# Kernel tuning notes

Hardware: AMD Instinct MI355X
Metric: run time of the kernel (lower is better)

The kernel has to match this reference:

```python
import jax, jax.numpy as jnp
import numpy as np

EPS = 1e-6
MAX_Q = 25.0
B, M, N, S = 1024, 8192, 32, 128


def setup_inputs() -> dict:
    key = jax.random.key(0)
    k = jax.random.split(key, 6)
    z = jax.random.normal(k[0], (B, N), jnp.float32) * 1e-3
    z_j = jax.random.uniform(k[1], (M, N), jnp.float32, -1e-3, 1e-3)
    vec_d_j = jax.random.uniform(k[2], (M, N), jnp.float32, -1e-3, 1e-3)
    T_hat_j = jax.random.uniform(k[3], (M, S), jnp.float32, -1e-3, 1e-3)
    alpha_j = jnp.ones((M,), jnp.float32)
    sigma_par = jax.random.uniform(k[4], (M,), jnp.float32, 0.9, 1.5)
    sigma_perp = jax.random.uniform(k[5], (M,), jnp.float32, 0.1, 0.8)
    return {"z": z, "z_j": z_j, "vec_d_j": vec_d_j, "T_hat_j": T_hat_j,
            "alpha_j": alpha_j, "sigma_par": sigma_par, "sigma_perp": sigma_perp}


def reference(z, z_j, vec_d_j, T_hat_j, alpha_j, sigma_par, sigma_perp):
    tiny = jnp.finfo(sigma_par.dtype).eps
    w_par = 1.0 / jnp.maximum(sigma_par, tiny) ** 2      # [M]
    w_perp = 1.0 / jnp.maximum(sigma_perp, tiny) ** 2    # [M]
    w_diff = w_par - w_perp                               # [M]

    dz = z[:, None, :] - z_j[None, :, :]                  # [B, M, N]
    dz_norm_sq = jnp.sum(dz * dz, axis=-1)                # [B, M]

    d_norm = jnp.linalg.norm(vec_d_j, axis=-1, keepdims=True)  # [M, 1]
    use_proj = (d_norm > EPS).astype(z.dtype)                   # [M, 1]
    b = jnp.where(d_norm > EPS, vec_d_j / d_norm, jnp.zeros_like(vec_d_j))  # [M, N]
    proj = jnp.einsum('bmn,mn->bm', dz, b) * use_proj[:, 0][None, :]        # [B, M]

    q_pos = w_perp[None, :] * dz_norm_sq + w_diff[None, :] * (proj * proj)  # [B, M]
    q_pos = jnp.minimum(q_pos, jnp.asarray(MAX_Q, dtype=z.dtype))

    gain = alpha_j[None, :] * jnp.exp(-jnp.pi * q_pos)    # [B, M]
    T = gain @ T_hat_j                                     # [B, S]
    return T
```

## Files before the change

kernel.cpp:

```cpp
#include <hip/hip_runtime.h>
#include <hip/hip_bf16.h>
#include <math.h>

#define B_SZ 1024
#define M_SZ 8192
#define N_SZ 32
#define S_SZ 128

#define MT   256
#define BT   64
#define NTHR 256

#define SG_STRIDE 264

typedef __bf16 bf16x8 __attribute__((ext_vector_type(8)));
typedef float  f32x4  __attribute__((ext_vector_type(4)));

#define NSPLIT 32
#define WS_TSWZ_BYTES  ((size_t)M_SZ * S_SZ * 2)
#define WS_PART_BYTES  ((size_t)NSPLIT * B_SZ * S_SZ * 4)
#define WS_NEED        (WS_TSWZ_BYTES + WS_PART_BYTES)

__global__ __launch_bounds__(256)
void prep_T_kernel(const float* __restrict__ T, char* __restrict__ Tswz)
{
    const int g    = blockIdx.x * 256 + threadIdx.x;
    const int mc   = g >> 9;
    const int ns   = (g >> 6) & 7;
    const int lane = g & 63;
    const int c    = lane & 15;
    const int q    = lane >> 4;
    const float* src = T + (size_t)(mc * 32 + q * 8) * S_SZ + ns * 16 + c;
    bf16x8 v;
    #pragma unroll
    for (int j = 0; j < 8; ++j) v[j] = (__bf16)src[(size_t)j * S_SZ];
    *(bf16x8*)(Tswz + (size_t)g * 16) = v;
}

__global__ __launch_bounds__(NTHR, 2)
void cpsf_mfma_kernel(const float* __restrict__ z,
                      const float* __restrict__ z_j,
                      const float* __restrict__ vec_d_j,
                      const char*  __restrict__ Tswz,
                      const float* __restrict__ alpha_j,
                      const float* __restrict__ sigma_par,
                      const float* __restrict__ sigma_perp,
                      float* __restrict__ ws_part)
{
    __shared__ __align__(16) float sZ[BT * N_SZ];
    __shared__ float sZn[BT];
    __shared__ __align__(16) __hip_bfloat16 sG[BT * SG_STRIDE];

    const int t     = threadIdx.x;
    const int mx    = blockIdx.x;
    const int m0    = mx * MT;
    const int bbase = blockIdx.y * BT;

    {
        const float4* z4 = (const float4*)z + (size_t)bbase * (N_SZ / 4);
        float4* s4 = (float4*)sZ;
        #pragma unroll
        for (int i = t; i < BT * N_SZ / 4; i += NTHR) s4[i] = z4[i];
    }

    const int m = m0 + t;
    float zj[N_SZ], dv[N_SZ];
    {
        const float4* a4 = (const float4*)(z_j     + (size_t)m * N_SZ);
        const float4* d4 = (const float4*)(vec_d_j + (size_t)m * N_SZ);
        #pragma unroll
        for (int i = 0; i < N_SZ / 4; ++i) {
            float4 av = a4[i], dw = d4[i];
            zj[4*i+0]=av.x; zj[4*i+1]=av.y; zj[4*i+2]=av.z; zj[4*i+3]=av.w;
            dv[4*i+0]=dw.x; dv[4*i+1]=dw.y; dv[4*i+2]=dw.z; dv[4*i+3]=dw.w;
        }
    }
    float zjn = 0.f, dnsq = 0.f, zjd = 0.f;
    #pragma unroll
    for (int n = 0; n < N_SZ; ++n) {
        zjn  += zj[n] * zj[n];
        dnsq += dv[n] * dv[n];
        zjd  += zj[n] * dv[n];
    }
    const float dn     = sqrtf(dnsq);
    const float inv_dn = (dn > 1e-6f) ? (1.0f / dn) : 0.0f;
    const float P0     = zjd * inv_dn;
    const float tiny   = 1.1920928955078125e-07f;
    const float sp  = fmaxf(sigma_par[m],  tiny);
    const float spp = fmaxf(sigma_perp[m], tiny);
    const float wpar  = 1.0f / (sp  * sp);
    const float wperp = 1.0f / (spp * spp);
    const float wdiff = wpar - wperp;
    const float Cc    = wperp * zjn;
    const float al    = alpha_j[m];

    __syncthreads();
    if (t < BT) {
        float s = 0.f;
        #pragma unroll
        for (int n = 0; n < N_SZ; ++n) { float v = sZ[t * N_SZ + n]; s += v * v; }
        sZn[t] = s;
    }
    __syncthreads();

    const float PI_F = 3.14159274101257324f;
    for (int b = 0; b < BT; ++b) {
        float s1 = 0.f, sd = 0.f;
        #pragma unroll
        for (int n = 0; n < N_SZ; ++n) {
            const float zv = sZ[b * N_SZ + n];
            s1 += zv * zj[n];
            sd += zv * dv[n];
        }
        const float p = sd * inv_dn - P0;
        float q = wperp * sZn[b] - 2.0f * wperp * s1 + Cc + wdiff * p * p;
        q = fminf(q, 25.0f);
        const float g = al * __expf(-PI_F * q);
        sG[b * SG_STRIDE + t] = __float2bfloat16(g);
    }
    __syncthreads();

    const int lane = t & 63;
    const int w    = t >> 6;
    const int q    = lane >> 4;
    const int c    = lane & 15;

    f32x4 acc[8];
    #pragma unroll
    for (int ns = 0; ns < 8; ++ns) acc[ns] = (f32x4){0.f, 0.f, 0.f, 0.f};

    const char* sGb = (const char*)sG + (size_t)(w * 16 + c) * (SG_STRIDE * 2);
    #pragma unroll
    for (int kc = 0; kc < MT / 32; ++kc) {
        bf16x8 a = *(const bf16x8*)(sGb + kc * 64 + q * 16);
        const int mc = mx * (MT / 32) + kc;
        #pragma unroll
        for (int ns = 0; ns < 8; ++ns) {
            bf16x8 b = *(const bf16x8*)(Tswz + ((size_t)(mc * 8 + ns) * 64 + lane) * 16);
            acc[ns] = __builtin_amdgcn_mfma_f32_16x16x32_bf16(a, b, acc[ns], 0, 0, 0);
        }
    }

    float* part = ws_part + (size_t)mx * (B_SZ * S_SZ)
                + (size_t)(bbase + w * 16 + q * 4) * S_SZ + c;
    #pragma unroll
    for (int ns = 0; ns < 8; ++ns)
        #pragma unroll
        for (int reg = 0; reg < 4; ++reg)
            part[(size_t)reg * S_SZ + ns * 16] = acc[ns][reg];
}

__global__ __launch_bounds__(256)
void reduce_kernel(const float* __restrict__ part, float* __restrict__ out)
{
    const int i = blockIdx.x * 256 + threadIdx.x;
    const f32x4* p = (const f32x4*)part;
    f32x4 s = p[i];
    #pragma unroll
    for (int sp = 1; sp < NSPLIT; ++sp) {
        f32x4 v = p[(size_t)sp * (B_SZ * S_SZ / 4) + i];
        s = s + v;
    }
    ((f32x4*)out)[i] = s;
}

#define SGF_STRIDE 68
__global__ __launch_bounds__(NTHR, 2)
void cpsf_fused_fallback(const float* __restrict__ z,
                         const float* __restrict__ z_j,
                         const float* __restrict__ vec_d_j,
                         const float* __restrict__ T_hat,
                         const float* __restrict__ alpha_j,
                         const float* __restrict__ sigma_par,
                         const float* __restrict__ sigma_perp,
                         float* __restrict__ out)
{
    __shared__ float sZ[BT * N_SZ];
    __shared__ float sZn[BT];
    __shared__ float sG[MT * SGF_STRIDE];

    const int t     = threadIdx.x;
    const int m0    = blockIdx.x * MT;
    const int bbase = blockIdx.y * BT;

    {
        const float4* z4 = (const float4*)z + (size_t)bbase * (N_SZ / 4);
        float4* s4 = (float4*)sZ;
        #pragma unroll
        for (int i = t; i < BT * N_SZ / 4; i += NTHR) s4[i] = z4[i];
    }
    const int m = m0 + t;
    float zj[N_SZ], dv[N_SZ];
    {
        const float4* a4 = (const float4*)(z_j     + (size_t)m * N_SZ);
        const float4* d4 = (const float4*)(vec_d_j + (size_t)m * N_SZ);
        #pragma unroll
        for (int i = 0; i < N_SZ / 4; ++i) {
            float4 av = a4[i], dw = d4[i];
            zj[4*i+0]=av.x; zj[4*i+1]=av.y; zj[4*i+2]=av.z; zj[4*i+3]=av.w;
            dv[4*i+0]=dw.x; dv[4*i+1]=dw.y; dv[4*i+2]=dw.z; dv[4*i+3]=dw.w;
        }
    }
    float zjn = 0.f, dnsq = 0.f, zjd = 0.f;
    #pragma unroll
    for (int n = 0; n < N_SZ; ++n) {
        zjn += zj[n]*zj[n]; dnsq += dv[n]*dv[n]; zjd += zj[n]*dv[n];
    }
    const float dn = sqrtf(dnsq);
    const float inv_dn = (dn > 1e-6f) ? (1.0f / dn) : 0.0f;
    const float P0 = zjd * inv_dn;
    const float tiny = 1.1920928955078125e-07f;
    const float sp  = fmaxf(sigma_par[m],  tiny);
    const float spp = fmaxf(sigma_perp[m], tiny);
    const float wperp = 1.0f / (spp * spp);
    const float wdiff = 1.0f / (sp * sp) - wperp;
    const float Cc = wperp * zjn;
    const float al = alpha_j[m];

    __syncthreads();
    if (t < BT) {
        float s = 0.f;
        #pragma unroll
        for (int n = 0; n < N_SZ; ++n) { float v = sZ[t*N_SZ+n]; s += v*v; }
        sZn[t] = s;
    }
    __syncthreads();

    const float PI_F = 3.14159274101257324f;
    for (int bq = 0; bq < BT / 4; ++bq) {
        float g[4];
        #pragma unroll
        for (int k = 0; k < 4; ++k) {
            const int b = bq*4 + k;
            float s1 = 0.f, sd = 0.f;
            #pragma unroll
            for (int n = 0; n < N_SZ; ++n) {
                const float zv = sZ[b*N_SZ+n];
                s1 += zv*zj[n]; sd += zv*dv[n];
            }
            const float p = sd*inv_dn - P0;
            float qv = wperp*sZn[b] - 2.0f*wperp*s1 + Cc + wdiff*p*p;
            qv = fminf(qv, 25.0f);
            g[k] = al * __expf(-PI_F*qv);
        }
        *(float4*)&sG[t*SGF_STRIDE + bq*4] = make_float4(g[0],g[1],g[2],g[3]);
    }
    __syncthreads();

    const int sg = t & 15, bg = t >> 4;
    const int b0 = bg*4, s0 = sg*8;
    float acc[4][8];
    #pragma unroll
    for (int i = 0; i < 4; ++i)
        #pragma unroll
        for (int j = 0; j < 8; ++j) acc[i][j] = 0.f;
    const float4* th4 = (const float4*)T_hat + (size_t)m0*(S_SZ/4) + sg*2;
    for (int mm = 0; mm < MT; ++mm) {
        const float4 g4 = *(const float4*)&sG[mm*SGF_STRIDE + b0];
        const float4 ta = th4[(size_t)mm*(S_SZ/4)];
        const float4 tb = th4[(size_t)mm*(S_SZ/4)+1];
        const float gg[4] = {g4.x,g4.y,g4.z,g4.w};
        const float tv[8] = {ta.x,ta.y,ta.z,ta.w,tb.x,tb.y,tb.z,tb.w};
        #pragma unroll
        for (int i = 0; i < 4; ++i)
            #pragma unroll
            for (int j = 0; j < 8; ++j) acc[i][j] += gg[i]*tv[j];
    }
    float* op = out + (size_t)(bbase + b0)*S_SZ + s0;
    #pragma unroll
    for (int i = 0; i < 4; ++i)
        #pragma unroll
        for (int j = 0; j < 8; ++j)
            unsafeAtomicAdd(&op[i*S_SZ + j], acc[i][j]);
}

extern "C" void kernel_launch(void* const* d_in, const int* in_sizes, int n_in,
                              void* d_out, int out_size, void* d_ws, size_t ws_size,
                              hipStream_t stream) {
    (void)in_sizes; (void)n_in; (void)out_size;

    const float* z          = (const float*)d_in[0];
    const float* z_j        = (const float*)d_in[1];
    const float* vec_d_j    = (const float*)d_in[2];
    const float* T_hat_j    = (const float*)d_in[3];
    const float* alpha_j    = (const float*)d_in[4];
    const float* sigma_par  = (const float*)d_in[5];
    const float* sigma_perp = (const float*)d_in[6];
    float* out = (float*)d_out;

    if (ws_size >= WS_NEED) {
        char*  Tswz = (char*)d_ws;
        float* part = (float*)((char*)d_ws + WS_TSWZ_BYTES);

        prep_T_kernel<<<dim3(M_SZ * S_SZ / (256 * 8)), 256, 0, stream>>>(T_hat_j, Tswz);

        dim3 grid(NSPLIT, B_SZ / BT);
        cpsf_mfma_kernel<<<grid, NTHR, 0, stream>>>(
            z, z_j, vec_d_j, Tswz, alpha_j, sigma_par, sigma_perp, part);

        reduce_kernel<<<dim3(B_SZ * S_SZ / (256 * 4)), 256, 0, stream>>>(part, out);
    } else {
        hipMemsetAsync(out, 0, (size_t)B_SZ * S_SZ * sizeof(float), stream);
        dim3 grid(M_SZ / MT, B_SZ / BT);
        cpsf_fused_fallback<<<grid, NTHR, 0, stream>>>(
            z, z_j, vec_d_j, T_hat_j, alpha_j, sigma_par, sigma_perp, out);
    }
}
```

Measured before the change: 107.3 us.

## Compute distance dot products with bf16 MFMA and precompute per-row constants in prep kernel

The prep kernel now also converts z, z_j and the normalised direction vectors to bf16 and precomputes the per-m constants (weights, norms, projection offset, alpha) and the per-b squared norms into workspace. The main kernel computes the z·z_j and z·d dot products with bf16 MFMA tiles instead of scalar FP32 loops over shared memory. The second GEMM is reorganised so each wave covers all 64 rows and a 32-column slice of S, and occupancy is raised to 4 blocks per CU. This removes the scalar VALU dot-product cost, but bf16 inputs to the quadratic form (a difference of near-equal terms) risk precision loss.

```diff
diff --git a/kernel.cpp b/kernel.cpp
--- a/kernel.cpp
+++ b/kernel.cpp
@@ -10,144 +10,191 @@
 #define MT   256
 #define BT   64
 #define NTHR 256
+#define NSPLIT 32
 
 #define SG_STRIDE 264
 
 typedef __bf16 bf16x8 __attribute__((ext_vector_type(8)));
 typedef float  f32x4  __attribute__((ext_vector_type(4)));
 
-#define NSPLIT 32
-#define WS_TSWZ_BYTES  ((size_t)M_SZ * S_SZ * 2)
-#define WS_PART_BYTES  ((size_t)NSPLIT * B_SZ * S_SZ * 4)
-#define WS_NEED        (WS_TSWZ_BYTES + WS_PART_BYTES)
+#define WS_TSWZ   ((size_t)0)
+#define WS_ZJBF   ((size_t)2 * 1024 * 1024)
+#define WS_DVBF   (WS_ZJBF + (size_t)M_SZ * N_SZ * 2)
+#define WS_MCONST (WS_DVBF + (size_t)M_SZ * N_SZ * 2)
+#define WS_ZBF    (WS_MCONST + (size_t)M_SZ * 8 * 4)
+#define WS_ZN     (WS_ZBF + (size_t)B_SZ * N_SZ * 2)
+#define WS_PART   ((size_t)4 * 1024 * 1024)
+#define WS_NEED   (WS_PART + (size_t)NSPLIT * B_SZ * S_SZ * 4)
 
 __global__ __launch_bounds__(256)
-void prep_T_kernel(const float* __restrict__ T, char* __restrict__ Tswz)
+void prep_kernel(const float* __restrict__ T,
+                 const float* __restrict__ z,
+                 const float* __restrict__ zj_in,
+                 const float* __restrict__ dv_in,
+                 const float* __restrict__ alpha_j,
+                 const float* __restrict__ sigma_par,
+                 const float* __restrict__ sigma_perp,
+                 char* __restrict__ ws)
 {
-    const int g    = blockIdx.x * 256 + threadIdx.x;
-    const int mc   = g >> 9;
-    const int ns   = (g >> 6) & 7;
-    const int lane = g & 63;
-    const int c    = lane & 15;
-    const int q    = lane >> 4;
-    const float* src = T + (size_t)(mc * 32 + q * 8) * S_SZ + ns * 16 + c;
-    bf16x8 v;
-    #pragma unroll
-    for (int j = 0; j < 8; ++j) v[j] = (__bf16)src[(size_t)j * S_SZ];
-    *(bf16x8*)(Tswz + (size_t)g * 16) = v;
-}
-
-__global__ __launch_bounds__(NTHR, 2)
-void cpsf_mfma_kernel(const float* __restrict__ z,
-                      const float* __restrict__ z_j,
-                      const float* __restrict__ vec_d_j,
-                      const char*  __restrict__ Tswz,
-                      const float* __restrict__ alpha_j,
-                      const float* __restrict__ sigma_par,
-                      const float* __restrict__ sigma_perp,
-                      float* __restrict__ ws_part)
+    const int bx = blockIdx.x;
+    const int t  = threadIdx.x;
+
+    if (bx < 512) {
+        const int g    = bx * 256 + t;
+        const int mc   = g >> 9;
+        const int ns   = (g >> 6) & 7;
+        const int lane = g & 63;
+        const int c    = lane & 15;
+        const int q    = lane >> 4;
+        const float* src = T + (size_t)(mc * 32 + q * 8) * S_SZ + ns * 16 + c;
+        bf16x8 v;
+        #pragma unroll
+        for (int j = 0; j < 8; ++j) v[j] = (__bf16)src[(size_t)j * S_SZ];
+        *(bf16x8*)(ws + WS_TSWZ + (size_t)g * 16) = v;
+    } else if (bx < 544) {
+        const int m = (bx - 512) * 256 + t;
+        float a[N_SZ], d[N_SZ];
+        const float4* a4 = (const float4*)(zj_in + (size_t)m * N_SZ);
+        const float4* d4 = (const float4*)(dv_in + (size_t)m * N_SZ);
+        #pragma unroll
+        for (int i = 0; i < N_SZ / 4; ++i) {
+            float4 av = a4[i], dw = d4[i];
+            a[4*i+0]=av.x; a[4*i+1]=av.y; a[4*i+2]=av.z; a[4*i+3]=av.w;
+            d[4*i+0]=dw.x; d[4*i+1]=dw.y; d[4*i+2]=dw.z; d[4*i+3]=dw.w;
+        }
+        float zjn = 0.f, dnsq = 0.f, zjd = 0.f;
+        #pragma unroll
+        for (int n = 0; n < N_SZ; ++n) {
+            zjn += a[n]*a[n]; dnsq += d[n]*d[n]; zjd += a[n]*d[n];
+        }
+        const float dn  = sqrtf(dnsq);
+        const float inv = (dn > 1e-6f) ? (1.0f / dn) : 0.0f;
+        __bf16* zjb = (__bf16*)(ws + WS_ZJBF) + (size_t)m * N_SZ;
+        __bf16* dvb = (__bf16*)(ws + WS_DVBF) + (size_t)m * N_SZ;
+        #pragma unroll
+        for (int i = 0; i < 4; ++i) {
+            bf16x8 vz, vd;
+            #pragma unroll
+            for (int j = 0; j < 8; ++j) {
+                vz[j] = (__bf16)a[i*8+j];
+                vd[j] = (__bf16)(d[i*8+j] * inv);
+            }
+            *(bf16x8*)(zjb + i*8) = vz;
+            *(bf16x8*)(dvb + i*8) = vd;
+        }
+        const float tiny = 1.1920928955078125e-07f;
+        const float sp  = fmaxf(sigma_par[m],  tiny);
+        const float spp = fmaxf(sigma_perp[m], tiny);
+        const float wperp = 1.0f / (spp * spp);
+        const float wdiff = 1.0f / (sp * sp) - wperp;
+        float* mc8 = (float*)(ws + WS_MCONST) + (size_t)m * 8;
+        *(f32x4*)mc8       = (f32x4){wperp, wperp * zjn, wdiff, zjd * inv};
+        *(f32x4*)(mc8 + 4) = (f32x4){alpha_j[m], 0.f, 0.f, 0.f};
+    } else {
+        const int b = (bx - 544) * 256 + t;
+        float v[N_SZ];
+        const float4* z4 = (const float4*)(z + (size_t)b * N_SZ);
+        #pragma unroll
+        for (int i = 0; i < N_SZ / 4; ++i) {
+            float4 w4 = z4[i];
+            v[4*i+0]=w4.x; v[4*i+1]=w4.y; v[4*i+2]=w4.z; v[4*i+3]=w4.w;
+        }
+        float zn = 0.f;
+        #pragma unroll
+        for (int n = 0; n < N_SZ; ++n) zn += v[n]*v[n];
+        __bf16* zb = (__bf16*)(ws + WS_ZBF) + (size_t)b * N_SZ;
+        #pragma unroll
+        for (int i = 0; i < 4; ++i) {
+            bf16x8 vz;
+            #pragma unroll
+            for (int j = 0; j < 8; ++j) vz[j] = (__bf16)v[i*8+j];
+            *(bf16x8*)(zb + i*8) = vz;
+        }
+        ((float*)(ws + WS_ZN))[b] = zn;
+    }
+}
+
+__global__ __launch_bounds__(NTHR, 4)
+void cpsf_main_kernel(const char* __restrict__ ws_ro, float* __restrict__ ws_part)
 {
-    __shared__ __align__(16) float sZ[BT * N_SZ];
-    __shared__ float sZn[BT];
-    __shared__ __align__(16) __hip_bfloat16 sG[BT * SG_STRIDE];
+    __shared__ __align__(16) __bf16 sG[BT * SG_STRIDE];
 
     const int t     = threadIdx.x;
+    const int lane  = t & 63;
+    const int w     = t >> 6;
+    const int q     = lane >> 4;
+    const int c     = lane & 15;
     const int mx    = blockIdx.x;
     const int m0    = mx * MT;
     const int bbase = blockIdx.y * BT;
 
-    {
-        const float4* z4 = (const float4*)z + (size_t)bbase * (N_SZ / 4);
-        float4* s4 = (float4*)sZ;
-        #pragma unroll
-        for (int i = t; i < BT * N_SZ / 4; i += NTHR) s4[i] = z4[i];
-    }
-
-    const int m = m0 + t;
-    float zj[N_SZ], dv[N_SZ];
-    {
-        const float4* a4 = (const float4*)(z_j     + (size_t)m * N_SZ);
-        const float4* d4 = (const float4*)(vec_d_j + (size_t)m * N_SZ);
-        #pragma unroll
-        for (int i = 0; i < N_SZ / 4; ++i) {
-            float4 av = a4[i], dw = d4[i];
-            zj[4*i+0]=av.x; zj[4*i+1]=av.y; zj[4*i+2]=av.z; zj[4*i+3]=av.w;
-            dv[4*i+0]=dw.x; dv[4*i+1]=dw.y; dv[4*i+2]=dw.z; dv[4*i+3]=dw.w;
-        }
-    }
-    float zjn = 0.f, dnsq = 0.f, zjd = 0.f;
-    #pragma unroll
-    for (int n = 0; n < N_SZ; ++n) {
-        zjn  += zj[n] * zj[n];
-        dnsq += dv[n] * dv[n];
-        zjd  += zj[n] * dv[n];
-    }
-    const float dn     = sqrtf(dnsq);
-    const float inv_dn = (dn > 1e-6f) ? (1.0f / dn) : 0.0f;
-    const float P0     = zjd * inv_dn;
-    const float tiny   = 1.1920928955078125e-07f;
-    const float sp  = fmaxf(sigma_par[m],  tiny);
-    const float spp = fmaxf(sigma_perp[m], tiny);
-    const float wpar  = 1.0f / (sp  * sp);
-    const float wperp = 1.0f / (spp * spp);
-    const float wdiff = wpar - wperp;
-    const float Cc    = wperp * zjn;
-    const float al    = alpha_j[m];
-
+    const __bf16* zbf   = (const __bf16*)(ws_ro + WS_ZBF);
+    const __bf16* zjbf  = (const __bf16*)(ws_ro + WS_ZJBF);
+    const __bf16* dvbf  = (const __bf16*)(ws_ro + WS_DVBF);
+    const float*  mcst  = (const float*)(ws_ro + WS_MCONST);
+    const float*  znp   = (const float*)(ws_ro + WS_ZN);
+    const char*   Tswz  = ws_ro + WS_TSWZ;
+
+    const bf16x8 zA  = *(const bf16x8*)(zbf + ((size_t)(bbase + w*16 + c) * N_SZ + q*8));
+    const f32x4  zn4 = *(const f32x4*)(znp + bbase + w*16 + q*4);
+
+    const float PI_F = 3.14159274101257324f;
+    #pragma unroll 4
+    for (int tile = 0; tile < MT / 16; ++tile) {
+        const size_t boff = (size_t)(m0 + tile*16 + c) * N_SZ + q*8;
+        const bf16x8 bz = *(const bf16x8*)(zjbf + boff);
+        const bf16x8 bd = *(const bf16x8*)(dvbf + boff);
+        f32x4 s1 = __builtin_amdgcn_mfma_f32_16x16x32_bf16(zA, bz, (f32x4){0.f,0.f,0.f,0.f}, 0, 0, 0);
+        f32x4 sd = __builtin_amdgcn_mfma_f32_16x16x32_bf16(zA, bd, (f32x4){0.f,0.f,0.f,0.f}, 0, 0, 0);
+        const float* mc8 = mcst + (size_t)(m0 + tile*16 + c) * 8;
+        const f32x4 mc0 = *(const f32x4*)mc8;
+        const float al  = mc8[4];
+        #pragma unroll
+        for (int reg = 0; reg < 4; ++reg) {
+            const float t1 = fmaf(s1[reg], -2.0f, zn4[reg]);
+            float qv = fmaf(mc0[0], t1, mc0[1]);
+            const float p  = sd[reg] - mc0[3];
+            qv = fmaf(mc0[2] * p, p, qv);
+            qv = fminf(qv, 25.0f);
+            const float g = al * __expf(-PI_F * qv);
+            sG[(size_t)(w*16 + q*4 + reg) * SG_STRIDE + tile*16 + c] = (__bf16)g;
+        }
+    }
     __syncthreads();
-    if (t < BT) {
-        float s = 0.f;
-        #pragma unroll
-        for (int n = 0; n < N_SZ; ++n) { float v = sZ[t * N_SZ + n]; s += v * v; }
-        sZn[t] = s;
-    }
-    __syncthreads();
-
-    const float PI_F = 3.14159274101257324f;
-    for (int b = 0; b < BT; ++b) {
-        float s1 = 0.f, sd = 0.f;
-        #pragma unroll
-        for (int n = 0; n < N_SZ; ++n) {
-            const float zv = sZ[b * N_SZ + n];
-            s1 += zv * zj[n];
-            sd += zv * dv[n];
-        }
-        const float p = sd * inv_dn - P0;
-        float q = wperp * sZn[b] - 2.0f * wperp * s1 + Cc + wdiff * p * p;
-        q = fminf(q, 25.0f);
-        const float g = al * __expf(-PI_F * q);
-        sG[b * SG_STRIDE + t] = __float2bfloat16(g);
-    }
-    __syncthreads();
-
-    const int lane = t & 63;
-    const int w    = t >> 6;
-    const int q    = lane >> 4;
-    const int c    = lane & 15;
-
-    f32x4 acc[8];
-    #pragma unroll
-    for (int ns = 0; ns < 8; ++ns) acc[ns] = (f32x4){0.f, 0.f, 0.f, 0.f};
-
-    const char* sGb = (const char*)sG + (size_t)(w * 16 + c) * (SG_STRIDE * 2);
-    #pragma unroll
+
+    f32x4 acc[4][2];
+    #pragma unroll
+    for (int bt = 0; bt < 4; ++bt)
+        #pragma unroll
+        for (int i = 0; i < 2; ++i) acc[bt][i] = (f32x4){0.f,0.f,0.f,0.f};
+
+    #pragma unroll 2
     for (int kc = 0; kc < MT / 32; ++kc) {
-        bf16x8 a = *(const bf16x8*)(sGb + kc * 64 + q * 16);
         const int mc = mx * (MT / 32) + kc;
-        #pragma unroll
-        for (int ns = 0; ns < 8; ++ns) {
-            bf16x8 b = *(const bf16x8*)(Tswz + ((size_t)(mc * 8 + ns) * 64 + lane) * 16);
-            acc[ns] = __builtin_amdgcn_mfma_f32_16x16x32_bf16(a, b, acc[ns], 0, 0, 0);
-        }
-    }
-
-    float* part = ws_part + (size_t)mx * (B_SZ * S_SZ)
-                + (size_t)(bbase + w * 16 + q * 4) * S_SZ + c;
-    #pragma unroll
-    for (int ns = 0; ns < 8; ++ns)
-        #pragma unroll
-        for (int reg = 0; reg < 4; ++reg)
-            part[(size_t)reg * S_SZ + ns * 16] = acc[ns][reg];
+        bf16x8 bfr[2];
+        #pragma unroll
+        for (int i = 0; i < 2; ++i)
+            bfr[i] = *(const bf16x8*)(Tswz + ((size_t)(mc*8 + w*2 + i) * 64 + lane) * 16);
+        #pragma unroll
+        for (int bt = 0; bt < 4; ++bt) {
+            const bf16x8 a = *(const bf16x8*)((const char*)sG
+                              + (size_t)(bt*16 + c) * (SG_STRIDE*2) + kc*64 + q*16);
+            #pragma unroll
+            for (int i = 0; i < 2; ++i)
+                acc[bt][i] = __builtin_amdgcn_mfma_f32_16x16x32_bf16(a, bfr[i], acc[bt][i], 0, 0, 0);
+        }
+    }
+
+    #pragma unroll
+    for (int bt = 0; bt < 4; ++bt) {
+        float* part = ws_part + (size_t)mx * (B_SZ * S_SZ)
+                    + (size_t)(bbase + bt*16 + q*4) * S_SZ + w*32 + c;
+        #pragma unroll
+        for (int i = 0; i < 2; ++i)
+            #pragma unroll
+            for (int reg = 0; reg < 4; ++reg)
+                part[(size_t)reg * S_SZ + i*16] = acc[bt][i][reg];
+    }
 }
 
 __global__ __launch_bounds__(256)
@@ -157,10 +204,8 @@
     const f32x4* p = (const f32x4*)part;
     f32x4 s = p[i];
     #pragma unroll
-    for (int sp = 1; sp < NSPLIT; ++sp) {
-        f32x4 v = p[(size_t)sp * (B_SZ * S_SZ / 4) + i];
-        s = s + v;
-    }
+    for (int sp = 1; sp < NSPLIT; ++sp)
+        s = s + p[(size_t)sp * (B_SZ * S_SZ / 4) + i];
     ((f32x4*)out)[i] = s;
 }
 
@@ -289,14 +334,14 @@
     float* out = (float*)d_out;
 
     if (ws_size >= WS_NEED) {
-        char*  Tswz = (char*)d_ws;
-        float* part = (float*)((char*)d_ws + WS_TSWZ_BYTES);
-
-        prep_T_kernel<<<dim3(M_SZ * S_SZ / (256 * 8)), 256, 0, stream>>>(T_hat_j, Tswz);
+        char*  ws   = (char*)d_ws;
+        float* part = (float*)(ws + WS_PART);
+
+        prep_kernel<<<dim3(548), 256, 0, stream>>>(
+            T_hat_j, z, z_j, vec_d_j, alpha_j, sigma_par, sigma_perp, ws);
 
         dim3 grid(NSPLIT, B_SZ / BT);
-        cpsf_mfma_kernel<<<grid, NTHR, 0, stream>>>(
-            z, z_j, vec_d_j, Tswz, alpha_j, sigma_par, sigma_perp, part);
+        cpsf_main_kernel<<<grid, NTHR, 0, stream>>>(ws, part);
 
         reduce_kernel<<<dim3(B_SZ * S_SZ / (256 * 4)), 256, 0, stream>>>(part, out);
     } else {
```

New measurement: 94.95 us. 11.5% less time.
